# Kernel tuning notes

Hardware: AMD Instinct MI355X
Metric: run time of the kernel (lower is better)

Reference implementation:

```python
import jax, jax.numpy as jnp
import numpy as np

B, C, H, W = 4, 64, 64, 128


def setup_inputs() -> dict:
    key = jax.random.key(0)
    ks = jax.random.split(key, 10)
    s = 1.0 / np.sqrt(C)
    return {
        "query": jax.random.normal(ks[0], (B, C, H, W), dtype=jnp.float32),
        "key_": jax.random.normal(ks[1], (B, C, H, W), dtype=jnp.float32),
        "value": jax.random.normal(ks[2], (B, C, H, W), dtype=jnp.float32),
        "Wq": jax.random.normal(ks[3], (C, C), dtype=jnp.float32) * s,
        "bq": jax.random.normal(ks[4], (C,), dtype=jnp.float32) * s,
        "Wk": jax.random.normal(ks[5], (C, C), dtype=jnp.float32) * s,
        "bk": jax.random.normal(ks[6], (C,), dtype=jnp.float32) * s,
        "Wv": jax.random.normal(ks[7], (C, C), dtype=jnp.float32) * s,
        "bv": jax.random.normal(ks[8], (C,), dtype=jnp.float32) * s,
        "gamma": jax.random.normal(ks[9], (), dtype=jnp.float32) * 0.1,
    }


def reference(query, key_, value, Wq, bq, Wk, bk, Wv, bv, gamma):
    b, c, h, w = query.shape
    n = h * w
    fq = query.reshape(b, c, n)
    fk = key_.reshape(b, c, n)
    fv = value.reshape(b, c, n)
    # 1x1 Conv1d == per-position channel matmul: [C_out, C_in] x [B, C_in, N]
    q = jnp.einsum('oc,bcn->bon', Wq, fq) + bq[:, None]
    k = jnp.einsum('oc,bcn->bon', Wk, fk) + bk[:, None]
    v = jnp.einsum('oc,bcn->bon', Wv, fv) + bv[:, None]
    # query permuted to [B, N, C], bmm with key [B, C, N] -> [B, Nq, Nk]; scale by W (last dim of input shape)
    qk = jnp.einsum('bcn,bcm->bnm', q, k) / w
    # non-standard softmax over dim=1 (query-position axis)
    attn = jax.nn.softmax(qk, axis=1)
    # value [B, C, N] @ attn [B, Nq, Nk] -> [B, C, Nk]
    av = jnp.einsum('bcn,bnm->bcm', v, attn)
    out = gamma * av.reshape(b, c, h, w) + v.reshape(b, c, h, w)
    return out
```

## Files before the change

### kernel.cpp

```cpp
#include <hip/hip_runtime.h>

#define NPOS 8192
#define NC 64
#define NB 4
#define NSPLIT 3
#define NCHUNK 2752
#define QSCALE 0.01127105500167846f

typedef __bf16 bf16x8 __attribute__((ext_vector_type(8)));
typedef __bf16 bf16x4 __attribute__((ext_vector_type(4)));
typedef float f32x4 __attribute__((ext_vector_type(4)));

#define EXP2F(x) __builtin_amdgcn_exp2f(x)

static __device__ __forceinline__ unsigned f2bf_u(float x) {
  unsigned u = __float_as_uint(x);
  return (u + 0x7FFFu + ((u >> 16) & 1u)) >> 16;
}
static __device__ __forceinline__ unsigned pack2(float a, float b) {
  return f2bf_u(a) | (f2bf_u(b) << 16);
}

static __device__ __forceinline__ void gload_lds16(const void* gsrc, void* lds_base) {
  __builtin_amdgcn_global_load_lds(
      (const __attribute__((address_space(1))) unsigned int*)gsrc,
      (__attribute__((address_space(3))) unsigned int*)lds_base, 16, 0, 0);
}

__global__ __launch_bounds__(256) void proj_kernel(
    const float* __restrict__ xq, const float* __restrict__ xk, const float* __restrict__ xv,
    const float* __restrict__ Wq, const float* __restrict__ bq,
    const float* __restrict__ Wk, const float* __restrict__ bk,
    const float* __restrict__ Wv, const float* __restrict__ bv,
    unsigned short* __restrict__ qT, unsigned short* __restrict__ kT,
    unsigned short* __restrict__ vb, float* __restrict__ vf)
{
  __shared__ float sW[NC * NC];
  __shared__ float sB[NC];
  const int p = blockIdx.z, b = blockIdx.y;
  const int n0 = blockIdx.x * 128;
  const int tid = threadIdx.x;
  const int wv = tid >> 6, l = tid & 63;

  const float* x    = p == 0 ? xq : (p == 1 ? xk : xv);
  const float* W    = p == 0 ? Wq : (p == 1 ? Wk : Wv);
  const float* bias = p == 0 ? bq : (p == 1 ? bk : bv);

  for (int i = tid; i < NC * NC; i += 256) sW[i] = W[i];
  if (tid < NC) sB[tid] = bias[tid];
  __syncthreads();

  const int nb = n0 + 2 * l;
  const float* xb = x + (size_t)b * NC * NPOS + nb;

  float acc[16][2];
#pragma unroll
  for (int oi = 0; oi < 16; ++oi) {
    float bz = sB[16 * wv + oi];
    acc[oi][0] = bz; acc[oi][1] = bz;
  }
  for (int c = 0; c < NC; ++c) {
    const float2 x2 = *(const float2*)(xb + (size_t)c * NPOS);
#pragma unroll
    for (int oi = 0; oi < 16; ++oi) {
      float wgt = sW[(16 * wv + oi) * NC + c];
      acc[oi][0] = fmaf(wgt, x2.x, acc[oi][0]);
      acc[oi][1] = fmaf(wgt, x2.y, acc[oi][1]);
    }
  }

  if (p < 2) {
    const float qs = (p == 0) ? QSCALE : 1.0f;
    unsigned short* dst = (p == 0 ? qT : kT) + (size_t)b * NPOS * NC;
#pragma unroll
    for (int r = 0; r < 2; ++r) {
      uint4 w0, w1;
      w0.x = pack2(qs * acc[0][r],  qs * acc[1][r]);
      w0.y = pack2(qs * acc[2][r],  qs * acc[3][r]);
      w0.z = pack2(qs * acc[4][r],  qs * acc[5][r]);
      w0.w = pack2(qs * acc[6][r],  qs * acc[7][r]);
      w1.x = pack2(qs * acc[8][r],  qs * acc[9][r]);
      w1.y = pack2(qs * acc[10][r], qs * acc[11][r]);
      w1.z = pack2(qs * acc[12][r], qs * acc[13][r]);
      w1.w = pack2(qs * acc[14][r], qs * acc[15][r]);
      unsigned short* rp = dst + (size_t)(nb + r) * NC + 16 * wv;
      *(uint4*)(rp) = w0;
      *(uint4*)(rp + 8) = w1;
    }
  } else {
#pragma unroll
    for (int oi = 0; oi < 16; ++oi) {
      const int o = 16 * wv + oi;
      float2 v2;
      v2.x = acc[oi][0]; v2.y = acc[oi][1];
      *(float2*)(vf + ((size_t)b * NC + o) * NPOS + nb) = v2;
      *(unsigned*)(vb + ((size_t)b * NC + o) * NPOS + nb) = pack2(acc[oi][0], acc[oi][1]);
    }
  }
}

__global__ __launch_bounds__(512) void attn_partial(
    const unsigned short* __restrict__ qT,
    const unsigned short* __restrict__ kT,
    const unsigned short* __restrict__ vb,
    float* __restrict__ pav, float* __restrict__ plsum)
{
  __shared__ unsigned short qs_[2][64 * 64];
  __shared__ unsigned short vs_[2][64 * 64];
  __shared__ unsigned short pT[8][16][68];

  const int b = blockIdx.y, z = blockIdx.z;
  const int m0 = blockIdx.x * 128;
  const int tid = threadIdx.x;
  const int w = tid >> 6, l = tid & 63;
  const int lm = l & 15, g = l >> 4;
  const int m = m0 + 16 * w + lm;

  const unsigned short* kb_p = kT + (size_t)(b * NPOS + m) * NC + 8 * g;
  const bf16x8 kb0 = *(const bf16x8*)(kb_p);
  const bf16x8 kb1 = *(const bf16x8*)(kb_p + 32);

  const char* qb  = (const char*)(qT + (size_t)b * NPOS * NC);
  const char* vbb = (const char*)(vb + (size_t)b * NC * NPOS);

  const int srow = tid >> 3;
  const int slc  = ((tid & 7) * 16) ^ ((srow & 7) << 4);
  const char* qsrc0 = qb + (size_t)srow * 128 + slc;
  const char* vsrc0 = vbb + (size_t)srow * (NPOS * 2) + slc;
  const int ldsoff = w * 512;

  f32x4 acc[4] = {{0,0,0,0},{0,0,0,0},{0,0,0,0},{0,0,0,0}};
  float lsum = 0.f;

  const int nbeg = z * NCHUNK;
  const int nend = (nbeg + NCHUNK < NPOS) ? nbeg + NCHUNK : NPOS;
  const int iters = (nend - nbeg) >> 6;

  gload_lds16(qsrc0 + (size_t)nbeg * 128, &qs_[0][ldsoff]);
  gload_lds16(vsrc0 + (size_t)nbeg * 2,   &vs_[0][ldsoff]);

  const int swz = (lm & 7) << 4;

  int cur = 0;
  for (int t = 0; t < iters; ++t) {
    const int n0 = nbeg + 64 * t;
    __builtin_amdgcn_s_barrier();
    if (t + 1 < iters) {
      gload_lds16(qsrc0 + (size_t)(n0 + 64) * 128, &qs_[cur ^ 1][ldsoff]);
      gload_lds16(vsrc0 + (size_t)(n0 + 64) * 2,   &vs_[cur ^ 1][ldsoff]);
      asm volatile("s_waitcnt vmcnt(2)" ::: "memory");
    } else {
      asm volatile("s_waitcnt vmcnt(0)" ::: "memory");
    }
    __builtin_amdgcn_s_barrier();
    __builtin_amdgcn_sched_barrier(0);

    const unsigned short* qt = qs_[cur];
    const unsigned short* vt = vs_[cur];

    f32x4 s[4];
    __builtin_amdgcn_s_setprio(1);
#pragma unroll
    for (int sub = 0; sub < 4; ++sub) {
      const int nl = 16 * sub + lm;
      bf16x8 qa0 = *(const bf16x8*)(qt + nl * 64 + (((16 * g) ^ swz) >> 1));
      bf16x8 qa1 = *(const bf16x8*)(qt + nl * 64 + (((64 + 16 * g) ^ swz) >> 1));
      f32x4 zz = {0, 0, 0, 0};
      zz = __builtin_amdgcn_mfma_f32_16x16x32_bf16(qa0, kb0, zz, 0, 0, 0);
      zz = __builtin_amdgcn_mfma_f32_16x16x32_bf16(qa1, kb1, zz, 0, 0, 0);
      s[sub] = zz;
    }
    __builtin_amdgcn_s_setprio(0);
#pragma unroll
    for (int sub = 0; sub < 4; ++sub) {
      float p0 = EXP2F(s[sub][0]);
      float p1 = EXP2F(s[sub][1]);
      float p2 = EXP2F(s[sub][2]);
      float p3 = EXP2F(s[sub][3]);
      lsum += (p0 + p1) + (p2 + p3);
      bf16x4 pk;
      pk[0] = (__bf16)p0; pk[1] = (__bf16)p1;
      pk[2] = (__bf16)p2; pk[3] = (__bf16)p3;
      *(bf16x4*)&pT[w][lm][16 * sub + 4 * g] = pk;
    }
    __builtin_amdgcn_s_setprio(1);
#pragma unroll
    for (int ks = 0; ks < 2; ++ks) {
      bf16x8 pb = *(const bf16x8*)&pT[w][lm][8 * g + 32 * ks];
#pragma unroll
      for (int cs = 0; cs < 4; ++cs) {
        const int vr = 16 * cs + lm;
        bf16x8 va = *(const bf16x8*)(vt + vr * 64 + (((16 * g + 64 * ks) ^ swz) >> 1));
        acc[cs] = __builtin_amdgcn_mfma_f32_16x16x32_bf16(va, pb, acc[cs], 0, 0, 0);
      }
    }
    __builtin_amdgcn_s_setprio(0);
    cur ^= 1;
  }

  lsum += __shfl_xor(lsum, 16);
  lsum += __shfl_xor(lsum, 32);
  if (l < 16) plsum[((size_t)(z * NB + b) << 13) + m] = lsum;

  float* po = pav + ((size_t)((z * NB + b) * NC) << 13);
#pragma unroll
  for (int cs = 0; cs < 4; ++cs) {
#pragma unroll
    for (int r = 0; r < 4; ++r) {
      const int c = 16 * cs + 4 * g + r;
      po[((size_t)c << 13) + m] = acc[cs][r];
    }
  }
}

__global__ __launch_bounds__(256) void reduce_kernel(
    const float* __restrict__ pav, const float* __restrict__ plsum,
    const float* __restrict__ vf, const float* __restrict__ gamma_p,
    float* __restrict__ out)
{
  const size_t base = ((size_t)blockIdx.x * 256 + threadIdx.x) * 4;
  const int m = (int)(base & (NPOS - 1));
  const int bc = (int)(base >> 13);
  const int b = bc >> 6;

  float4 s = {0, 0, 0, 0};
  float4 L = {0, 0, 0, 0};
#pragma unroll
  for (int zz = 0; zz < NSPLIT; ++zz) {
    const float4 a = *(const float4*)(pav + (((size_t)(zz * NB * NC + bc)) << 13) + m);
    s.x += a.x; s.y += a.y; s.z += a.z; s.w += a.w;
    const float4 q = *(const float4*)(plsum + (((size_t)(zz * NB + b)) << 13) + m);
    L.x += q.x; L.y += q.y; L.z += q.z; L.w += q.w;
  }
  const float gmv = gamma_p[0];
  const float4 v4 = *(const float4*)(vf + base);
  float4 o;
  o.x = gmv * s.x / L.x + v4.x;
  o.y = gmv * s.y / L.y + v4.y;
  o.z = gmv * s.z / L.z + v4.z;
  o.w = gmv * s.w / L.w + v4.w;
  *(float4*)(out + base) = o;
}

extern "C" void kernel_launch(void* const* d_in, const int* in_sizes, int n_in,
                              void* d_out, int out_size, void* d_ws, size_t ws_size,
                              hipStream_t stream) {
  const float* xq = (const float*)d_in[0];
  const float* xk = (const float*)d_in[1];
  const float* xv = (const float*)d_in[2];
  const float* Wq = (const float*)d_in[3];
  const float* bq = (const float*)d_in[4];
  const float* Wk = (const float*)d_in[5];
  const float* bk = (const float*)d_in[6];
  const float* Wv = (const float*)d_in[7];
  const float* bv = (const float*)d_in[8];
  const float* gm = (const float*)d_in[9];
  float* out = (float*)d_out;

  unsigned short* qT   = (unsigned short*)d_ws;
  unsigned short* kT   = qT + (size_t)NB * NPOS * NC;
  unsigned short* vbuf = kT + (size_t)NB * NPOS * NC;
  float* vf    = (float*)(vbuf + (size_t)NB * NPOS * NC);
  float* pav   = vf + (size_t)NB * NC * NPOS;
  float* plsum = pav + (size_t)NSPLIT * NB * NC * NPOS;

  hipLaunchKernelGGL(proj_kernel, dim3(64, 4, 3), dim3(256), 0, stream,
                     xq, xk, xv, Wq, bq, Wk, bk, Wv, bv, qT, kT, vbuf, vf);
  hipLaunchKernelGGL(attn_partial, dim3(NPOS / 128, NB, NSPLIT), dim3(512), 0, stream,
                     qT, kT, vbuf, pav, plsum);
  hipLaunchKernelGGL(reduce_kernel, dim3(2048), dim3(256), 0, stream,
                     pav, plsum, vf, gm, out);
}
```

Baseline: 115.2 us.

## Process two key tiles per wave to reuse Q/V LDS tiles, split into four chunks

Each wave now computes attention for two 16-column key tiles, reusing the loaded Q and V fragments for both, which halves the Q/V global and LDS loading per output column. The grid is reshaped to 256 columns per block and the query axis is split into four equal chunks instead of three uneven ones. This raises register pressure and reduces the number of blocks, and the reduction must sum one more partial buffer.

```diff
diff --git a/kernel.cpp b/kernel.cpp
--- a/kernel.cpp
+++ b/kernel.cpp
@@ -3,8 +3,8 @@
 #define NPOS 8192
 #define NC 64
 #define NB 4
-#define NSPLIT 3
-#define NCHUNK 2752
+#define NSPLIT 4
+#define NCHUNK 2048
 #define QSCALE 0.01127105500167846f
 
 typedef __bf16 bf16x8 __attribute__((ext_vector_type(8)));
@@ -99,7 +99,7 @@
   }
 }
 
-__global__ __launch_bounds__(512) void attn_partial(
+__global__ __launch_bounds__(512, 4) void attn_partial(
     const unsigned short* __restrict__ qT,
     const unsigned short* __restrict__ kT,
     const unsigned short* __restrict__ vb,
@@ -110,15 +110,19 @@
   __shared__ unsigned short pT[8][16][68];
 
   const int b = blockIdx.y, z = blockIdx.z;
-  const int m0 = blockIdx.x * 128;
+  const int m0 = blockIdx.x * 256;
   const int tid = threadIdx.x;
   const int w = tid >> 6, l = tid & 63;
   const int lm = l & 15, g = l >> 4;
-  const int m = m0 + 16 * w + lm;
-
-  const unsigned short* kb_p = kT + (size_t)(b * NPOS + m) * NC + 8 * g;
-  const bf16x8 kb0 = *(const bf16x8*)(kb_p);
-  const bf16x8 kb1 = *(const bf16x8*)(kb_p + 32);
+  const int mA = m0 + 32 * w + lm;
+  const int mB = mA + 16;
+
+  const unsigned short* kbA = kT + (size_t)(b * NPOS + mA) * NC + 8 * g;
+  const unsigned short* kbB = kT + (size_t)(b * NPOS + mB) * NC + 8 * g;
+  const bf16x8 kb0 = *(const bf16x8*)(kbA);
+  const bf16x8 kb1 = *(const bf16x8*)(kbA + 32);
+  const bf16x8 kb2 = *(const bf16x8*)(kbB);
+  const bf16x8 kb3 = *(const bf16x8*)(kbB + 32);
 
   const char* qb  = (const char*)(qT + (size_t)b * NPOS * NC);
   const char* vbb = (const char*)(vb + (size_t)b * NC * NPOS);
@@ -129,12 +133,12 @@
   const char* vsrc0 = vbb + (size_t)srow * (NPOS * 2) + slc;
   const int ldsoff = w * 512;
 
-  f32x4 acc[4] = {{0,0,0,0},{0,0,0,0},{0,0,0,0},{0,0,0,0}};
-  float lsum = 0.f;
+  f32x4 accA[4] = {{0,0,0,0},{0,0,0,0},{0,0,0,0},{0,0,0,0}};
+  f32x4 accB[4] = {{0,0,0,0},{0,0,0,0},{0,0,0,0},{0,0,0,0}};
+  float lsumA = 0.f, lsumB = 0.f;
 
   const int nbeg = z * NCHUNK;
-  const int nend = (nbeg + NCHUNK < NPOS) ? nbeg + NCHUNK : NPOS;
-  const int iters = (nend - nbeg) >> 6;
+  const int iters = NCHUNK >> 6;
 
   gload_lds16(qsrc0 + (size_t)nbeg * 128, &qs_[0][ldsoff]);
   gload_lds16(vsrc0 + (size_t)nbeg * 2,   &vs_[0][ldsoff]);
@@ -158,31 +162,37 @@
     const unsigned short* qt = qs_[cur];
     const unsigned short* vt = vs_[cur];
 
-    f32x4 s[4];
+    f32x4 s0[4], s1[4];
     __builtin_amdgcn_s_setprio(1);
 #pragma unroll
     for (int sub = 0; sub < 4; ++sub) {
       const int nl = 16 * sub + lm;
       bf16x8 qa0 = *(const bf16x8*)(qt + nl * 64 + (((16 * g) ^ swz) >> 1));
       bf16x8 qa1 = *(const bf16x8*)(qt + nl * 64 + (((64 + 16 * g) ^ swz) >> 1));
-      f32x4 zz = {0, 0, 0, 0};
-      zz = __builtin_amdgcn_mfma_f32_16x16x32_bf16(qa0, kb0, zz, 0, 0, 0);
-      zz = __builtin_amdgcn_mfma_f32_16x16x32_bf16(qa1, kb1, zz, 0, 0, 0);
-      s[sub] = zz;
+      f32x4 za = {0, 0, 0, 0};
+      za = __builtin_amdgcn_mfma_f32_16x16x32_bf16(qa0, kb0, za, 0, 0, 0);
+      za = __builtin_amdgcn_mfma_f32_16x16x32_bf16(qa1, kb1, za, 0, 0, 0);
+      s0[sub] = za;
+      f32x4 zb = {0, 0, 0, 0};
+      zb = __builtin_amdgcn_mfma_f32_16x16x32_bf16(qa0, kb2, zb, 0, 0, 0);
+      zb = __builtin_amdgcn_mfma_f32_16x16x32_bf16(qa1, kb3, zb, 0, 0, 0);
+      s1[sub] = zb;
     }
     __builtin_amdgcn_s_setprio(0);
+
 #pragma unroll
     for (int sub = 0; sub < 4; ++sub) {
-      float p0 = EXP2F(s[sub][0]);
-      float p1 = EXP2F(s[sub][1]);
-      float p2 = EXP2F(s[sub][2]);
-      float p3 = EXP2F(s[sub][3]);
-      lsum += (p0 + p1) + (p2 + p3);
+      float p0 = EXP2F(s0[sub][0]);
+      float p1 = EXP2F(s0[sub][1]);
+      float p2 = EXP2F(s0[sub][2]);
+      float p3 = EXP2F(s0[sub][3]);
+      lsumA += (p0 + p1) + (p2 + p3);
       bf16x4 pk;
       pk[0] = (__bf16)p0; pk[1] = (__bf16)p1;
       pk[2] = (__bf16)p2; pk[3] = (__bf16)p3;
       *(bf16x4*)&pT[w][lm][16 * sub + 4 * g] = pk;
     }
+    bf16x8 va[2][4];
     __builtin_amdgcn_s_setprio(1);
 #pragma unroll
     for (int ks = 0; ks < 2; ++ks) {
@@ -190,17 +200,45 @@
 #pragma unroll
       for (int cs = 0; cs < 4; ++cs) {
         const int vr = 16 * cs + lm;
-        bf16x8 va = *(const bf16x8*)(vt + vr * 64 + (((16 * g + 64 * ks) ^ swz) >> 1));
-        acc[cs] = __builtin_amdgcn_mfma_f32_16x16x32_bf16(va, pb, acc[cs], 0, 0, 0);
+        va[ks][cs] = *(const bf16x8*)(vt + vr * 64 + (((16 * g + 64 * ks) ^ swz) >> 1));
+        accA[cs] = __builtin_amdgcn_mfma_f32_16x16x32_bf16(va[ks][cs], pb, accA[cs], 0, 0, 0);
+      }
+    }
+    __builtin_amdgcn_s_setprio(0);
+
+#pragma unroll
+    for (int sub = 0; sub < 4; ++sub) {
+      float p0 = EXP2F(s1[sub][0]);
+      float p1 = EXP2F(s1[sub][1]);
+      float p2 = EXP2F(s1[sub][2]);
+      float p3 = EXP2F(s1[sub][3]);
+      lsumB += (p0 + p1) + (p2 + p3);
+      bf16x4 pk;
+      pk[0] = (__bf16)p0; pk[1] = (__bf16)p1;
+      pk[2] = (__bf16)p2; pk[3] = (__bf16)p3;
+      *(bf16x4*)&pT[w][lm][16 * sub + 4 * g] = pk;
+    }
+    __builtin_amdgcn_s_setprio(1);
+#pragma unroll
+    for (int ks = 0; ks < 2; ++ks) {
+      bf16x8 pb = *(const bf16x8*)&pT[w][lm][8 * g + 32 * ks];
+#pragma unroll
+      for (int cs = 0; cs < 4; ++cs) {
+        accB[cs] = __builtin_amdgcn_mfma_f32_16x16x32_bf16(va[ks][cs], pb, accB[cs], 0, 0, 0);
       }
     }
     __builtin_amdgcn_s_setprio(0);
     cur ^= 1;
   }
 
-  lsum += __shfl_xor(lsum, 16);
-  lsum += __shfl_xor(lsum, 32);
-  if (l < 16) plsum[((size_t)(z * NB + b) << 13) + m] = lsum;
+  lsumA += __shfl_xor(lsumA, 16);
+  lsumA += __shfl_xor(lsumA, 32);
+  lsumB += __shfl_xor(lsumB, 16);
+  lsumB += __shfl_xor(lsumB, 32);
+  if (l < 16) {
+    plsum[((size_t)(z * NB + b) << 13) + mA] = lsumA;
+    plsum[((size_t)(z * NB + b) << 13) + mB] = lsumB;
+  }
 
   float* po = pav + ((size_t)((z * NB + b) * NC) << 13);
 #pragma unroll
@@ -208,7 +246,8 @@
 #pragma unroll
     for (int r = 0; r < 4; ++r) {
       const int c = 16 * cs + 4 * g + r;
-      po[((size_t)c << 13) + m] = acc[cs][r];
+      po[((size_t)c << 13) + mA] = accA[cs][r];
+      po[((size_t)c << 13) + mB] = accB[cs][r];
     }
   }
 }
@@ -266,7 +305,7 @@
 
   hipLaunchKernelGGL(proj_kernel, dim3(64, 4, 3), dim3(256), 0, stream,
                      xq, xk, xv, Wq, bq, Wk, bk, Wv, bv, qT, kT, vbuf, vf);
-  hipLaunchKernelGGL(attn_partial, dim3(NPOS / 128, NB, NSPLIT), dim3(512), 0, stream,
+  hipLaunchKernelGGL(attn_partial, dim3(NPOS / 256, NB, NSPLIT), dim3(512), 0, stream,
                      qT, kT, vbuf, pav, plsum);
   hipLaunchKernelGGL(reduce_kernel, dim3(2048), dim3(256), 0, stream,
                      pav, plsum, vf, gm, out);
```

Result: faster. 109.2 us (-5.2%).
